# Kernel tuning notes

Hardware: AMD Instinct MI355X
Metric: run time of the kernel (lower is better)

## Reference

```python
import jax, jax.numpy as jnp
import numpy as np

B, T, V, F = 8, 12, 2048, 16
K_CHEB, C = 3, 64

def setup_inputs() -> dict:
    key = jax.random.key(0)
    k1, k2, k3, k4 = jax.random.split(key, 4)
    x = jax.random.normal(k1, (B, T, V, F), dtype=jnp.float32)
    Att = jax.random.uniform(k2, (B, V, V), dtype=jnp.float32)
    cheb = jax.random.normal(k3, (K_CHEB, V, V), dtype=jnp.float32) / np.sqrt(V)
    theta = jax.random.normal(k4, (K_CHEB, F, C), dtype=jnp.float32) * 0.05
    return {"x": x, "Att": Att, "cheb": cheb, "theta": theta}

def reference(x, Att, cheb, theta):
    # Attention-masked Chebyshev polynomials: S_k[b,u,v] = T_k[u,v] * Att[b,u,v]
    # (dropout from the original training-time call is omitted: eval mode)
    masked = cheb[:, None, :, :] * Att[None, :, :, :]            # (K,B,V,V)
    # rhs[b,v,f] = sum_u S_k[b,u,v] * x[b,t,u,f]  (transpose+batch_dot)
    rhs = jnp.einsum('kbuv,btuf->kbtvf', masked, x)              # (K,B,T,V,F)
    # sum over Chebyshev order k of rhs @ Theta_k, then relu
    out = jnp.einsum('kbtvf,kfc->btvc', rhs, theta)              # (B,T,V,C)
    return jax.nn.relu(out)
```

## Files before the change

kernel.cpp:

```cpp
#include <hip/hip_runtime.h>
#include <hip/hip_bf16.h>
#include <stdint.h>

#define B_  8
#define T_  12
#define V_  2048
#define F_  16
#define K_  3
#define C_  64
#define N_  192

typedef _Float16 f16;
typedef _Float16 half4v __attribute__((ext_vector_type(4)));
typedef _Float16 half8v __attribute__((ext_vector_type(8)));
typedef float    f32x4  __attribute__((ext_vector_type(4)));
typedef float    f32x16 __attribute__((ext_vector_type(16)));
typedef unsigned int u32;

__global__ __launch_bounds__(256) void prep_xt(const float* __restrict__ x,
                                               f16* __restrict__ XT) {
  int bid = blockIdx.x;
  int bt = bid >> 2, uc = bid & 3;
  int b = bt / T_, t = bt % T_;
  __shared__ float tile[64][17];
  int r  = threadIdx.x >> 2, fq = threadIdx.x & 3;
  int f  = threadIdx.x >> 4, uq = threadIdx.x & 15;
  for (int u0 = uc * 512; u0 < uc * 512 + 512; u0 += 64) {
    f32x4 v = *(const f32x4*)(x + ((size_t)(b * T_ + t) * V_ + u0 + r) * F_ + fq * 4);
    tile[r][fq * 4 + 0] = v[0];
    tile[r][fq * 4 + 1] = v[1];
    tile[r][fq * 4 + 2] = v[2];
    tile[r][fq * 4 + 3] = v[3];
    __syncthreads();
    half4v h;
    h[0] = (f16)tile[uq * 4 + 0][f];
    h[1] = (f16)tile[uq * 4 + 1][f];
    h[2] = (f16)tile[uq * 4 + 2][f];
    h[3] = (f16)tile[uq * 4 + 3][f];
    *(half4v*)(XT + (size_t)(b * N_ + t * F_ + f) * V_ + u0 + uq * 4) = h;
    __syncthreads();
  }
}

__global__ __launch_bounds__(256) void gemm_kbv(const float* __restrict__ Att,
                                                const float* __restrict__ cheb,
                                                const f16* __restrict__ XT,
                                                f16* __restrict__ rhs) {
  const int vt = blockIdx.x & 31;
  const int kb = blockIdx.x >> 5;
  const int k = kb >> 3, b = kb & 7;
  const int vbase = vt * 64;

  __shared__ char smem[32768];
  char* Ab = smem;
  char* Bb = smem + 8192;

  const int tid = threadIdx.x;
  const int wave = tid >> 6, lane = tid & 63;
  const int wm = wave >> 1, wn = wave & 1;
  const int vsub = (tid & 15) * 4, usub = (tid >> 4) * 4;

  f32x16 acc[3];
  acc[0] = 0; acc[1] = 0; acc[2] = 0;

  for (int u0 = 0; u0 < V_; u0 += 64) {
    __syncthreads();
    const float* cp = cheb + ((size_t)k * V_ + u0 + usub) * V_ + vbase + vsub;
    const float* ap = Att  + ((size_t)b * V_ + u0 + usub) * V_ + vbase + vsub;
    f32x4 p[4];
#pragma unroll
    for (int i = 0; i < 4; ++i) {
      f32x4 cv = *(const f32x4*)(cp + (size_t)i * V_);
      f32x4 av = *(const f32x4*)(ap + (size_t)i * V_);
      p[i] = cv * av;
    }
#pragma unroll
    for (int j = 0; j < 4; ++j) {
      int vrow = vsub + j;
      half4v h;
      h[0] = (f16)p[0][j]; h[1] = (f16)p[1][j];
      h[2] = (f16)p[2][j]; h[3] = (f16)p[3][j];
      *(half4v*)(Ab + vrow * 128 + ((usub * 2) ^ ((vrow & 7) << 4))) = h;
    }
#pragma unroll
    for (int e = 0; e < 6; ++e) {
      int slot = wave * 6 + e;
      int n = slot * 8 + (lane >> 3);
      int cp2 = lane & 7;
      int c = cp2 ^ (n & 7);
      const f16* src = XT + (size_t)(b * N_ + n) * V_ + u0 + c * 8;
      __builtin_amdgcn_global_load_lds((const __attribute__((address_space(1))) u32*)src,
                                       (__attribute__((address_space(3))) u32*)(Bb + slot * 1024),
                                       16, 0, 0);
    }
    __syncthreads();
#pragma unroll
    for (int ks = 0; ks < 4; ++ks) {
      int koff = ks * 32 + (lane >> 5) * 16;
      int vrow = wm * 32 + (lane & 31);
      half8v a = *(const half8v*)(Ab + vrow * 128 + (koff ^ ((vrow & 7) << 4)));
#pragma unroll
      for (int nf = 0; nf < 3; ++nf) {
        int nrow = wn * 96 + nf * 32 + (lane & 31);
        half8v bv = *(const half8v*)(Bb + nrow * 128 + (koff ^ ((nrow & 7) << 4)));
        acc[nf] = __builtin_amdgcn_mfma_f32_32x32x16_f16(a, bv, acc[nf], 0, 0, 0);
      }
    }
  }

#pragma unroll
  for (int nf = 0; nf < 3; ++nf) {
    int n = wn * 96 + nf * 32 + (lane & 31);
    int t = n >> 4, fi = n & 15;
#pragma unroll
    for (int r = 0; r < 16; ++r) {
      int v = vbase + wm * 32 + (r & 3) + 8 * (r >> 2) + 4 * (lane >> 5);
      rhs[((size_t)(b * T_ + t) * V_ + v) * 48 + k * 16 + fi] = (f16)acc[nf][r];
    }
  }
}

__global__ __launch_bounds__(256) void epi(const f16* __restrict__ rhs,
                                           const float* __restrict__ theta,
                                           float* __restrict__ out) {
  int wave = threadIdx.x >> 6, lane = threadIdx.x & 63;
  int row0 = blockIdx.x * 128 + wave * 32;
  int cl = lane & 31, kh = (lane >> 5) * 8;

  half8v bf[2][3];
#pragma unroll
  for (int nf = 0; nf < 2; ++nf)
#pragma unroll
    for (int ks = 0; ks < 3; ++ks) {
      half8v hb;
#pragma unroll
      for (int j = 0; j < 8; ++j)
        hb[j] = (f16)theta[(size_t)(ks * 16 + kh + j) * C_ + nf * 32 + cl];
      bf[nf][ks] = hb;
    }

  f32x16 acc0 = 0, acc1 = 0;
#pragma unroll
  for (int ks = 0; ks < 3; ++ks) {
    half8v a = *(const half8v*)(rhs + (size_t)(row0 + cl) * 48 + ks * 16 + kh);
    acc0 = __builtin_amdgcn_mfma_f32_32x32x16_f16(a, bf[0][ks], acc0, 0, 0, 0);
    acc1 = __builtin_amdgcn_mfma_f32_32x32x16_f16(a, bf[1][ks], acc1, 0, 0, 0);
  }
#pragma unroll
  for (int r = 0; r < 16; ++r) {
    int row = row0 + (r & 3) + 8 * (r >> 2) + 4 * (lane >> 5);
    out[(size_t)row * C_ + cl]      = fmaxf(acc0[r], 0.f);
    out[(size_t)row * C_ + 32 + cl] = fmaxf(acc1[r], 0.f);
  }
}

extern "C" void kernel_launch(void* const* d_in, const int* in_sizes, int n_in,
                              void* d_out, int out_size, void* d_ws, size_t ws_size,
                              hipStream_t stream) {
  const float* x     = (const float*)d_in[0];
  const float* Att   = (const float*)d_in[1];
  const float* cheb  = (const float*)d_in[2];
  const float* theta = (const float*)d_in[3];
  float* out = (float*)d_out;

  f16* XT  = (f16*)d_ws;
  f16* rhs = (f16*)((char*)d_ws + (size_t)B_ * N_ * V_ * sizeof(f16));

  prep_xt<<<B_ * T_ * 4, 256, 0, stream>>>(x, XT);
  gemm_kbv<<<K_ * B_ * 32, 256, 0, stream>>>(Att, cheb, XT, rhs);
  epi<<<(B_ * T_ * V_) / 128, 256, 0, stream>>>(rhs, theta, out);
}
```

Measured before the change: 115.8 us.

## Double-buffer LDS tiles and prefetch next u-chunk during MFMA in gemm_kbv

Converts the main GEMM loop into a two-stage software pipeline. LDS doubles to 64KB so the next chunk's cheb/Att loads and XT global_load_lds run while the current chunk's MFMAs execute, leaving one barrier per iteration. It also reorders the block index so b is the fastest-varying dimension, which may improve L2 reuse of cheb across batches, and raises wave priority around the MFMA section. The larger LDS footprint and extra registers can lower occupancy.

```diff
diff --git a/kernel.cpp b/kernel.cpp
--- a/kernel.cpp
+++ b/kernel.cpp
@@ -46,66 +46,114 @@
                                                 const float* __restrict__ cheb,
                                                 const f16* __restrict__ XT,
                                                 f16* __restrict__ rhs) {
-  const int vt = blockIdx.x & 31;
-  const int kb = blockIdx.x >> 5;
-  const int k = kb >> 3, b = kb & 7;
+  const int bid = blockIdx.x;
+  const int b = bid & 7;
+  const int r2 = bid >> 3;
+  const int vt = r2 & 31, k = r2 >> 5;
   const int vbase = vt * 64;
 
-  __shared__ char smem[32768];
-  char* Ab = smem;
-  char* Bb = smem + 8192;
+  __shared__ char smem[65536];
 
   const int tid = threadIdx.x;
   const int wave = tid >> 6, lane = tid & 63;
   const int wm = wave >> 1, wn = wave & 1;
   const int vsub = (tid & 15) * 4, usub = (tid >> 4) * 4;
 
+  const float* cheb_base = cheb + (size_t)k * V_ * V_ + vbase + vsub + (size_t)usub * V_;
+  const float* att_base  = Att  + (size_t)b * V_ * V_ + vbase + vsub + (size_t)usub * V_;
+  const f16*   xt_base   = XT + (size_t)b * N_ * V_;
+
   f32x16 acc[3];
   acc[0] = 0; acc[1] = 0; acc[2] = 0;
 
-  for (int u0 = 0; u0 < V_; u0 += 64) {
-    __syncthreads();
-    const float* cp = cheb + ((size_t)k * V_ + u0 + usub) * V_ + vbase + vsub;
-    const float* ap = Att  + ((size_t)b * V_ + u0 + usub) * V_ + vbase + vsub;
-    f32x4 p[4];
-#pragma unroll
-    for (int i = 0; i < 4; ++i) {
-      f32x4 cv = *(const f32x4*)(cp + (size_t)i * V_);
-      f32x4 av = *(const f32x4*)(ap + (size_t)i * V_);
-      p[i] = cv * av;
-    }
+  f32x4 pc[4], pa[4];
+
+#pragma unroll
+  for (int i = 0; i < 4; ++i) {
+    pc[i] = *(const f32x4*)(cheb_base + (size_t)i * V_);
+    pa[i] = *(const f32x4*)(att_base  + (size_t)i * V_);
+  }
+  {
+    char* Bb = smem + 8192;
+#pragma unroll
+    for (int e = 0; e < 6; ++e) {
+      int slot = wave * 6 + e;
+      int n = slot * 8 + (lane >> 3);
+      int c = (lane & 7) ^ (n & 7);
+      const f16* src = xt_base + (size_t)n * V_ + c * 8;
+      __builtin_amdgcn_global_load_lds((const __attribute__((address_space(1))) u32*)src,
+                                       (__attribute__((address_space(3))) u32*)(Bb + slot * 1024),
+                                       16, 0, 0);
+    }
+    char* Ab = smem;
 #pragma unroll
     for (int j = 0; j < 4; ++j) {
       int vrow = vsub + j;
       half4v h;
-      h[0] = (f16)p[0][j]; h[1] = (f16)p[1][j];
-      h[2] = (f16)p[2][j]; h[3] = (f16)p[3][j];
+      h[0] = (f16)(pc[0][j] * pa[0][j]); h[1] = (f16)(pc[1][j] * pa[1][j]);
+      h[2] = (f16)(pc[2][j] * pa[2][j]); h[3] = (f16)(pc[3][j] * pa[3][j]);
       *(half4v*)(Ab + vrow * 128 + ((usub * 2) ^ ((vrow & 7) << 4))) = h;
     }
-#pragma unroll
-    for (int e = 0; e < 6; ++e) {
-      int slot = wave * 6 + e;
-      int n = slot * 8 + (lane >> 3);
-      int cp2 = lane & 7;
-      int c = cp2 ^ (n & 7);
-      const f16* src = XT + (size_t)(b * N_ + n) * V_ + u0 + c * 8;
-      __builtin_amdgcn_global_load_lds((const __attribute__((address_space(1))) u32*)src,
-                                       (__attribute__((address_space(3))) u32*)(Bb + slot * 1024),
-                                       16, 0, 0);
+  }
+  __syncthreads();
+
+  int cur = 0;
+  for (int t = 0; t < 32; ++t) {
+    char* bufc = smem + cur * 32768;
+    char* bufn = smem + (cur ^ 1) * 32768;
+
+    if (t < 31) {
+      const size_t uoff = (size_t)(t + 1) * 64 * V_;
+#pragma unroll
+      for (int i = 0; i < 4; ++i) {
+        pc[i] = *(const f32x4*)(cheb_base + uoff + (size_t)i * V_);
+        pa[i] = *(const f32x4*)(att_base  + uoff + (size_t)i * V_);
+      }
+      char* Bb = bufn + 8192;
+#pragma unroll
+      for (int e = 0; e < 6; ++e) {
+        int slot = wave * 6 + e;
+        int n = slot * 8 + (lane >> 3);
+        int c = (lane & 7) ^ (n & 7);
+        const f16* src = xt_base + (size_t)n * V_ + (t + 1) * 64 + c * 8;
+        __builtin_amdgcn_global_load_lds((const __attribute__((address_space(1))) u32*)src,
+                                         (__attribute__((address_space(3))) u32*)(Bb + slot * 1024),
+                                         16, 0, 0);
+      }
+    }
+
+    {
+      char* Ab = bufc;
+      char* Bb = bufc + 8192;
+      __builtin_amdgcn_s_setprio(1);
+#pragma unroll
+      for (int ks = 0; ks < 4; ++ks) {
+        int koff = ks * 32 + (lane >> 5) * 16;
+        int vrow = wm * 32 + (lane & 31);
+        half8v a = *(const half8v*)(Ab + vrow * 128 + (koff ^ ((vrow & 7) << 4)));
+#pragma unroll
+        for (int nf = 0; nf < 3; ++nf) {
+          int nrow = wn * 96 + nf * 32 + (lane & 31);
+          half8v bv = *(const half8v*)(Bb + nrow * 128 + (koff ^ ((nrow & 7) << 4)));
+          acc[nf] = __builtin_amdgcn_mfma_f32_32x32x16_f16(a, bv, acc[nf], 0, 0, 0);
+        }
+      }
+      __builtin_amdgcn_s_setprio(0);
+    }
+
+    if (t < 31) {
+      char* Ab = bufn;
+#pragma unroll
+      for (int j = 0; j < 4; ++j) {
+        int vrow = vsub + j;
+        half4v h;
+        h[0] = (f16)(pc[0][j] * pa[0][j]); h[1] = (f16)(pc[1][j] * pa[1][j]);
+        h[2] = (f16)(pc[2][j] * pa[2][j]); h[3] = (f16)(pc[3][j] * pa[3][j]);
+        *(half4v*)(Ab + vrow * 128 + ((usub * 2) ^ ((vrow & 7) << 4))) = h;
+      }
     }
     __syncthreads();
-#pragma unroll
-    for (int ks = 0; ks < 4; ++ks) {
-      int koff = ks * 32 + (lane >> 5) * 16;
-      int vrow = wm * 32 + (lane & 31);
-      half8v a = *(const half8v*)(Ab + vrow * 128 + (koff ^ ((vrow & 7) << 4)));
-#pragma unroll
-      for (int nf = 0; nf < 3; ++nf) {
-        int nrow = wn * 96 + nf * 32 + (lane & 31);
-        half8v bv = *(const half8v*)(Bb + nrow * 128 + (koff ^ ((nrow & 7) << 4)));
-        acc[nf] = __builtin_amdgcn_mfma_f32_32x32x16_f16(a, bv, acc[nf], 0, 0, 0);
-      }
-    }
+    cur ^= 1;
   }
 
 #pragma unroll
```

After: 140.3 us. +21.1%, slower.

## Fuse Chebyshev orders per block, split-K over u, and software-pipeline loads

Applied to the files above, without the earlier changes.

The GEMM kernel now handles all three Chebyshev orders in one block, so each Att tile and each XT tile is loaded once and reused across k instead of three times. The reduction over u is split into halves across blocks for parallelism. The epilogue sums the partials, which doubles the rhs intermediate. Next-step global loads are prefetched into registers during MFMA work, with setprio around the MFMA bursts. This raises register and LDS use (9 accumulators, 48KB LDS) and may cut occupancy.

```diff
diff --git a/kernel.cpp b/kernel.cpp
--- a/kernel.cpp
+++ b/kernel.cpp
@@ -42,84 +42,169 @@
   }
 }
 
-__global__ __launch_bounds__(256) void gemm_kbv(const float* __restrict__ Att,
-                                                const float* __restrict__ cheb,
-                                                const f16* __restrict__ XT,
-                                                f16* __restrict__ rhs) {
-  const int vt = blockIdx.x & 31;
-  const int kb = blockIdx.x >> 5;
-  const int k = kb >> 3, b = kb & 7;
+template<int UH>
+__global__ __launch_bounds__(256, 2) void gemm_fused(const float* __restrict__ Att,
+                                                     const float* __restrict__ cheb,
+                                                     const f16* __restrict__ XT,
+                                                     f16* __restrict__ rhs) {
+  constexpr int NSTEP = (V_ / UH) / 64;
+  const int bid = blockIdx.x;
+  const int b  = bid / (32 * UH);
+  const int rr = bid % (32 * UH);
+  const int vt = rr / UH, uh = rr % UH;
   const int vbase = vt * 64;
-
-  __shared__ char smem[32768];
+  const size_t ubase = (size_t)uh * (V_ / UH);
+
+  __shared__ char smem[49152];
   char* Ab = smem;
-  char* Bb = smem + 8192;
+  char* Bb = smem + 24576;
 
   const int tid = threadIdx.x;
   const int wave = tid >> 6, lane = tid & 63;
   const int wm = wave >> 1, wn = wave & 1;
   const int vsub = (tid & 15) * 4, usub = (tid >> 4) * 4;
 
-  f32x16 acc[3];
-  acc[0] = 0; acc[1] = 0; acc[2] = 0;
-
-  for (int u0 = 0; u0 < V_; u0 += 64) {
-    __syncthreads();
-    const float* cp = cheb + ((size_t)k * V_ + u0 + usub) * V_ + vbase + vsub;
-    const float* ap = Att  + ((size_t)b * V_ + u0 + usub) * V_ + vbase + vsub;
-    f32x4 p[4];
-#pragma unroll
-    for (int i = 0; i < 4; ++i) {
-      f32x4 cv = *(const f32x4*)(cp + (size_t)i * V_);
-      f32x4 av = *(const f32x4*)(ap + (size_t)i * V_);
-      p[i] = cv * av;
-    }
-#pragma unroll
-    for (int j = 0; j < 4; ++j) {
-      int vrow = vsub + j;
-      half4v h;
-      h[0] = (f16)p[0][j]; h[1] = (f16)p[1][j];
-      h[2] = (f16)p[2][j]; h[3] = (f16)p[3][j];
-      *(half4v*)(Ab + vrow * 128 + ((usub * 2) ^ ((vrow & 7) << 4))) = h;
-    }
+  const float* attb  = Att + (size_t)b * V_ * V_ + vbase + vsub + (size_t)usub * V_;
+  const float* chebb = cheb + vbase + vsub + (size_t)usub * V_;
+  const f16*   xtb   = XT + (size_t)b * N_ * V_;
+
+  f32x16 acc[3][3];
+#pragma unroll
+  for (int k = 0; k < 3; ++k)
+#pragma unroll
+    for (int nf = 0; nf < 3; ++nf) acc[k][nf] = 0;
+
+  const int vrow = wm * 32 + (lane & 31);
+  const int akey = ((vrow >> 2) & 7) << 4;
+  int nrowA[3], bkeyA[3];
+#pragma unroll
+  for (int nf = 0; nf < 3; ++nf) {
+    nrowA[nf] = wn * 96 + nf * 32 + (lane & 31);
+    bkeyA[nf] = (nrowA[nf] & 7) << 4;
+  }
+  const int wkey = (tid & 7) << 4;
+  const int gl_c = (lane & 7) ^ (lane >> 3);
+
+  auto stageB = [&](size_t u) {
 #pragma unroll
     for (int e = 0; e < 6; ++e) {
       int slot = wave * 6 + e;
       int n = slot * 8 + (lane >> 3);
-      int cp2 = lane & 7;
-      int c = cp2 ^ (n & 7);
-      const f16* src = XT + (size_t)(b * N_ + n) * V_ + u0 + c * 8;
+      const f16* src = xtb + (size_t)n * V_ + u + gl_c * 8;
       __builtin_amdgcn_global_load_lds((const __attribute__((address_space(1))) u32*)src,
                                        (__attribute__((address_space(3))) u32*)(Bb + slot * 1024),
                                        16, 0, 0);
     }
-    __syncthreads();
-#pragma unroll
-    for (int ks = 0; ks < 4; ++ks) {
-      int koff = ks * 32 + (lane >> 5) * 16;
-      int vrow = wm * 32 + (lane & 31);
-      half8v a = *(const half8v*)(Ab + vrow * 128 + (koff ^ ((vrow & 7) << 4)));
-#pragma unroll
-      for (int nf = 0; nf < 3; ++nf) {
-        int nrow = wn * 96 + nf * 32 + (lane & 31);
-        half8v bv = *(const half8v*)(Bb + nrow * 128 + (koff ^ ((nrow & 7) << 4)));
-        acc[nf] = __builtin_amdgcn_mfma_f32_32x32x16_f16(a, bv, acc[nf], 0, 0, 0);
+  };
+  auto writeA = [&](half4v pk[3][4]) {
+#pragma unroll
+    for (int k = 0; k < 3; ++k)
+#pragma unroll
+      for (int j = 0; j < 4; ++j)
+        *(half4v*)(Ab + k * 8192 + (vsub + j) * 128 + ((usub * 2) ^ wkey)) = pk[k][j];
+  };
+
+  {
+    f32x4 pa[4], cv[3][4];
+#pragma unroll
+    for (int i = 0; i < 4; ++i) pa[i] = *(const f32x4*)(attb + (ubase + i) * V_);
+#pragma unroll
+    for (int k = 0; k < 3; ++k)
+#pragma unroll
+      for (int i = 0; i < 4; ++i)
+        cv[k][i] = *(const f32x4*)(chebb + (size_t)k * V_ * V_ + (ubase + i) * V_);
+    stageB(ubase);
+    half4v pk[3][4];
+#pragma unroll
+    for (int k = 0; k < 3; ++k)
+#pragma unroll
+      for (int j = 0; j < 4; ++j) {
+        half4v h;
+        h[0] = (f16)(cv[k][0][j] * pa[0][j]); h[1] = (f16)(cv[k][1][j] * pa[1][j]);
+        h[2] = (f16)(cv[k][2][j] * pa[2][j]); h[3] = (f16)(cv[k][3][j] * pa[3][j]);
+        pk[k][j] = h;
       }
-    }
-  }
+    writeA(pk);
+    __syncthreads();
+  }
+
+#define COMPUTE_KS(ks)                                                          \
+  {                                                                             \
+    const int ku2 = (ks) * 32 + (lane >> 5) * 16;                               \
+    half8v bfr0 = *(const half8v*)(Bb + nrowA[0] * 128 + (ku2 ^ bkeyA[0]));     \
+    half8v bfr1 = *(const half8v*)(Bb + nrowA[1] * 128 + (ku2 ^ bkeyA[1]));     \
+    half8v bfr2 = *(const half8v*)(Bb + nrowA[2] * 128 + (ku2 ^ bkeyA[2]));     \
+    __builtin_amdgcn_s_setprio(1);                                              \
+    _Pragma("unroll")                                                           \
+    for (int k = 0; k < 3; ++k) {                                               \
+      half8v a = *(const half8v*)(Ab + k * 8192 + vrow * 128 + (ku2 ^ akey));   \
+      acc[k][0] = __builtin_amdgcn_mfma_f32_32x32x16_f16(a, bfr0, acc[k][0], 0, 0, 0); \
+      acc[k][1] = __builtin_amdgcn_mfma_f32_32x32x16_f16(a, bfr1, acc[k][1], 0, 0, 0); \
+      acc[k][2] = __builtin_amdgcn_mfma_f32_32x32x16_f16(a, bfr2, acc[k][2], 0, 0, 0); \
+    }                                                                           \
+    __builtin_amdgcn_s_setprio(0);                                              \
+  }
+
+  for (int t = 0; t < NSTEP; ++t) {
+    const bool pref = (t + 1) < NSTEP;
+    const size_t unext = ubase + (size_t)(t + 1) * 64;
+    f32x4 pa[4], cv[3][4];
+    half4v pk[3][4];
+
+    if (pref) {
+#pragma unroll
+      for (int i = 0; i < 4; ++i) pa[i] = *(const f32x4*)(attb + (unext + i) * V_);
+#pragma unroll
+      for (int k = 0; k < 3; ++k)
+#pragma unroll
+        for (int i = 0; i < 4; ++i)
+          cv[k][i] = *(const f32x4*)(chebb + (size_t)k * V_ * V_ + (unext + i) * V_);
+    }
+
+    COMPUTE_KS(0)
+    COMPUTE_KS(1)
+
+    if (pref) {
+#pragma unroll
+      for (int k = 0; k < 3; ++k)
+#pragma unroll
+        for (int j = 0; j < 4; ++j) {
+          half4v h;
+          h[0] = (f16)(cv[k][0][j] * pa[0][j]); h[1] = (f16)(cv[k][1][j] * pa[1][j]);
+          h[2] = (f16)(cv[k][2][j] * pa[2][j]); h[3] = (f16)(cv[k][3][j] * pa[3][j]);
+          pk[k][j] = h;
+        }
+    }
+
+    COMPUTE_KS(2)
+    COMPUTE_KS(3)
+
+    __syncthreads();
+    if (pref) {
+      stageB(unext);
+      writeA(pk);
+      __syncthreads();
+    }
+  }
+#undef COMPUTE_KS
 
 #pragma unroll
   for (int nf = 0; nf < 3; ++nf) {
     int n = wn * 96 + nf * 32 + (lane & 31);
-    int t = n >> 4, fi = n & 15;
-#pragma unroll
-    for (int r = 0; r < 16; ++r) {
-      int v = vbase + wm * 32 + (r & 3) + 8 * (r >> 2) + 4 * (lane >> 5);
-      rhs[((size_t)(b * T_ + t) * V_ + v) * 48 + k * 16 + fi] = (f16)acc[nf][r];
-    }
-  }
-}
-
+    int tt = n >> 4, fi = n & 15;
+#pragma unroll
+    for (int k = 0; k < 3; ++k) {
+#pragma unroll
+      for (int r = 0; r < 16; ++r) {
+        int v = vbase + wm * 32 + (r & 3) + 8 * (r >> 2) + 4 * (lane >> 5);
+        rhs[((size_t)(b * T_ + tt) * V_ + v) * (48 * UH) + uh * 48 + k * 16 + fi] =
+            (f16)acc[k][nf][r];
+      }
+    }
+  }
+}
+
+template<int UH>
 __global__ __launch_bounds__(256) void epi(const f16* __restrict__ rhs,
                                            const float* __restrict__ theta,
                                            float* __restrict__ out) {
@@ -141,10 +226,10 @@
 
   f32x16 acc0 = 0, acc1 = 0;
 #pragma unroll
-  for (int ks = 0; ks < 3; ++ks) {
-    half8v a = *(const half8v*)(rhs + (size_t)(row0 + cl) * 48 + ks * 16 + kh);
-    acc0 = __builtin_amdgcn_mfma_f32_32x32x16_f16(a, bf[0][ks], acc0, 0, 0, 0);
-    acc1 = __builtin_amdgcn_mfma_f32_32x32x16_f16(a, bf[1][ks], acc1, 0, 0, 0);
+  for (int s = 0; s < 3 * UH; ++s) {
+    half8v a = *(const half8v*)(rhs + (size_t)(row0 + cl) * (48 * UH) + s * 16 + kh);
+    acc0 = __builtin_amdgcn_mfma_f32_32x32x16_f16(a, bf[0][s % 3], acc0, 0, 0, 0);
+    acc1 = __builtin_amdgcn_mfma_f32_32x32x16_f16(a, bf[1][s % 3], acc1, 0, 0, 0);
   }
 #pragma unroll
   for (int r = 0; r < 16; ++r) {
@@ -163,10 +248,18 @@
   const float* theta = (const float*)d_in[3];
   float* out = (float*)d_out;
 
+  const size_t xtB   = (size_t)B_ * N_ * V_ * sizeof(f16);
+  const size_t rhsB2 = (size_t)B_ * T_ * V_ * 96 * sizeof(f16);
+
   f16* XT  = (f16*)d_ws;
-  f16* rhs = (f16*)((char*)d_ws + (size_t)B_ * N_ * V_ * sizeof(f16));
+  f16* rhs = (f16*)((char*)d_ws + xtB);
 
   prep_xt<<<B_ * T_ * 4, 256, 0, stream>>>(x, XT);
-  gemm_kbv<<<K_ * B_ * 32, 256, 0, stream>>>(Att, cheb, XT, rhs);
-  epi<<<(B_ * T_ * V_) / 128, 256, 0, stream>>>(rhs, theta, out);
-}
+  if (ws_size >= xtB + rhsB2) {
+    gemm_fused<2><<<B_ * 32 * 2, 256, 0, stream>>>(Att, cheb, XT, rhs);
+    epi<2><<<(B_ * T_ * V_) / 128, 256, 0, stream>>>(rhs, theta, out);
+  } else {
+    gemm_fused<1><<<B_ * 32, 256, 0, stream>>>(Att, cheb, XT, rhs);
+    epi<1><<<(B_ * T_ * V_) / 128, 256, 0, stream>>>(rhs, theta, out);
+  }
+}
```

After: 107.2 us. 7.5% less time.

## Share Att tiles across Chebyshev orders with split-U double-buffered GEMM

Applied to the files above, without the earlier changes.

The GEMM is restructured so each block loads its Att tile once and reuses it for all three Chebyshev orders, holding nine accumulators instead of three, which removes the threefold re-reading of Att. Cheb is pre-converted by a new kernel into an f16 layout that matches the MFMA register fragments, and is read straight from global memory and multiplied with the Att fragment in registers. The U dimension is split across two blocks and the partial sums are reduced in the epilogue GEMM, and the LDS staging is double-buffered so loads overlap with MFMA work. In exchange there is an extra prep pass over cheb, a larger workspace, and higher register and LDS pressure that limit occupancy.

```diff
diff --git a/kernel.cpp b/kernel.cpp
--- a/kernel.cpp
+++ b/kernel.cpp
@@ -42,84 +42,192 @@
   }
 }
 
-__global__ __launch_bounds__(256) void gemm_kbv(const float* __restrict__ Att,
-                                                const float* __restrict__ cheb,
+__global__ __launch_bounds__(256) void prep_chebT(const float* __restrict__ c,
+                                                  f16* __restrict__ cT) {
+  int bid = blockIdx.x;
+  int vt = bid & 31, ut = (bid >> 5) & 31, k = bid >> 10;
+  int u0 = ut * 64, v0 = vt * 64;
+  __shared__ float tile[64][68];
+  int tid = threadIdx.x;
+  int lr = tid >> 4, lc = (tid & 15) * 4;
+  const float* src = c + ((size_t)k * V_ + u0) * V_ + v0;
+#pragma unroll
+  for (int i = 0; i < 4; ++i) {
+    f32x4 v = *(const f32x4*)(src + (size_t)(lr + 16 * i) * V_ + lc);
+    tile[lr + 16 * i][lc + 0] = v[0];
+    tile[lr + 16 * i][lc + 1] = v[1];
+    tile[lr + 16 * i][lc + 2] = v[2];
+    tile[lr + 16 * i][lc + 3] = v[3];
+  }
+  __syncthreads();
+  int vl = tid & 63, uc0 = tid >> 6;
+#pragma unroll
+  for (int i = 0; i < 2; ++i) {
+    int uc = uc0 + 4 * i;
+    half8v h;
+#pragma unroll
+    for (int j = 0; j < 8; ++j) h[j] = (f16)tile[uc * 8 + j][vl];
+    int vb = (v0 + vl) >> 5;
+    int vi = vl & 31;
+    size_t ut_idx = (size_t)(u0 >> 3) + uc;
+    size_t off = ((((size_t)k * 64 + vb) * 256 + ut_idx) * 32 + vi) * 8;
+    *(half8v*)(cT + off) = h;
+  }
+}
+
+#define MFMA_H(a, b, c) __builtin_amdgcn_mfma_f32_32x32x16_f16(a, b, c, 0, 0, 0)
+
+#define KS_GROUP(ks, AC, BC)                                                   \
+  {                                                                            \
+    const int kb = (ks) * 32 + hi * 16;                                        \
+    half8v af = *(const half8v*)((AC) + vrow * 128 + (kb ^ skey));             \
+    half8v b0 = *(const half8v*)((BC) + nrow0 * 128 + (kb ^ bk0));             \
+    half8v b1 = *(const half8v*)((BC) + nrow1 * 128 + (kb ^ bk1));             \
+    half8v b2 = *(const half8v*)((BC) + nrow2 * 128 + (kb ^ bk2));             \
+    const size_t co = (size_t)(t * 8 + (ks) * 2 + hi) * 256;                   \
+    half8v c0 = *(const half8v*)(chb0 + co);                                   \
+    half8v c1 = *(const half8v*)(chb1 + co);                                   \
+    half8v c2 = *(const half8v*)(chb2 + co);                                   \
+    half8v a0 = c0 * af, a1 = c1 * af, a2 = c2 * af;                           \
+    __builtin_amdgcn_s_setprio(1);                                             \
+    acc[0][0] = MFMA_H(a0, b0, acc[0][0]);                                     \
+    acc[0][1] = MFMA_H(a0, b1, acc[0][1]);                                     \
+    acc[0][2] = MFMA_H(a0, b2, acc[0][2]);                                     \
+    acc[1][0] = MFMA_H(a1, b0, acc[1][0]);                                     \
+    acc[1][1] = MFMA_H(a1, b1, acc[1][1]);                                     \
+    acc[1][2] = MFMA_H(a1, b2, acc[1][2]);                                     \
+    acc[2][0] = MFMA_H(a2, b0, acc[2][0]);                                     \
+    acc[2][1] = MFMA_H(a2, b1, acc[2][1]);                                     \
+    acc[2][2] = MFMA_H(a2, b2, acc[2][2]);                                     \
+    __builtin_amdgcn_s_setprio(0);                                             \
+  }
+
+template<int UH>
+__global__ __launch_bounds__(256, 2) void gemm2(const float* __restrict__ Att,
+                                                const f16* __restrict__ chebT,
                                                 const f16* __restrict__ XT,
                                                 f16* __restrict__ rhs) {
-  const int vt = blockIdx.x & 31;
-  const int kb = blockIdx.x >> 5;
-  const int k = kb >> 3, b = kb & 7;
+  constexpr int NSTEP = (V_ / UH) / 64;
+  const int bid = blockIdx.x;
+  const int vt = bid & 31;
+  const int rr = bid >> 5;
+  const int b  = rr / UH;
+  const int uh = rr % UH;
   const int vbase = vt * 64;
-
-  __shared__ char smem[32768];
-  char* Ab = smem;
-  char* Bb = smem + 8192;
+  const size_t ubase = (size_t)uh * (V_ / UH);
+
+  __shared__ char smem[65536];
+  char* Bb0 = smem;
+  char* Bb1 = smem + 24576;
+  char* Ab0 = smem + 49152;
+  char* Ab1 = smem + 57344;
 
   const int tid = threadIdx.x;
   const int wave = tid >> 6, lane = tid & 63;
   const int wm = wave >> 1, wn = wave & 1;
+  const int hi = lane >> 5, l31 = lane & 31;
+  const int vrow = wm * 32 + l31;
   const int vsub = (tid & 15) * 4, usub = (tid >> 4) * 4;
 
-  f32x16 acc[3];
-  acc[0] = 0; acc[1] = 0; acc[2] = 0;
-
-  for (int u0 = 0; u0 < V_; u0 += 64) {
-    __syncthreads();
-    const float* cp = cheb + ((size_t)k * V_ + u0 + usub) * V_ + vbase + vsub;
-    const float* ap = Att  + ((size_t)b * V_ + u0 + usub) * V_ + vbase + vsub;
-    f32x4 p[4];
-#pragma unroll
-    for (int i = 0; i < 4; ++i) {
-      f32x4 cv = *(const f32x4*)(cp + (size_t)i * V_);
-      f32x4 av = *(const f32x4*)(ap + (size_t)i * V_);
-      p[i] = cv * av;
-    }
-#pragma unroll
-    for (int j = 0; j < 4; ++j) {
-      int vrow = vsub + j;
-      half4v h;
-      h[0] = (f16)p[0][j]; h[1] = (f16)p[1][j];
-      h[2] = (f16)p[2][j]; h[3] = (f16)p[3][j];
-      *(half4v*)(Ab + vrow * 128 + ((usub * 2) ^ ((vrow & 7) << 4))) = h;
-    }
+  const int skey = ((vrow + (vrow >> 3)) & 7) << 4;
+  const int nrow0 = wn * 96 + l31;
+  const int nrow1 = nrow0 + 32;
+  const int nrow2 = nrow0 + 64;
+  const int bk0 = (nrow0 & 7) << 4, bk1 = (nrow1 & 7) << 4, bk2 = (nrow2 & 7) << 4;
+
+  const int vb = vt * 2 + wm;
+  const f16* chb0 = chebT + (((size_t)vb * 256 + (ubase >> 3)) * 32 + l31) * 8;
+  const f16* chb1 = chb0 + (size_t)V_ * V_;
+  const f16* chb2 = chb1 + (size_t)V_ * V_;
+
+  const float* attb = Att + (size_t)b * V_ * V_ + (ubase + usub) * V_ + vbase + vsub;
+  const f16*   xtb  = XT + (size_t)b * N_ * V_ + ubase;
+
+  f32x16 acc[3][3];
+#pragma unroll
+  for (int k = 0; k < 3; ++k)
+#pragma unroll
+    for (int nf = 0; nf < 3; ++nf) acc[k][nf] = 0;
+
+  f32x4 pa[4];
+  const int gl_c = lane & 7;
+
+  auto stageB = [&](int t, char* Bb) {
 #pragma unroll
     for (int e = 0; e < 6; ++e) {
       int slot = wave * 6 + e;
       int n = slot * 8 + (lane >> 3);
-      int cp2 = lane & 7;
-      int c = cp2 ^ (n & 7);
-      const f16* src = XT + (size_t)(b * N_ + n) * V_ + u0 + c * 8;
+      int cc = gl_c ^ (n & 7);
+      const f16* src = xtb + (size_t)n * V_ + t * 64 + cc * 8;
       __builtin_amdgcn_global_load_lds((const __attribute__((address_space(1))) u32*)src,
                                        (__attribute__((address_space(3))) u32*)(Bb + slot * 1024),
                                        16, 0, 0);
     }
-    __syncthreads();
-#pragma unroll
-    for (int ks = 0; ks < 4; ++ks) {
-      int koff = ks * 32 + (lane >> 5) * 16;
-      int vrow = wm * 32 + (lane & 31);
-      half8v a = *(const half8v*)(Ab + vrow * 128 + (koff ^ ((vrow & 7) << 4)));
-#pragma unroll
-      for (int nf = 0; nf < 3; ++nf) {
-        int nrow = wn * 96 + nf * 32 + (lane & 31);
-        half8v bv = *(const half8v*)(Bb + nrow * 128 + (koff ^ ((nrow & 7) << 4)));
-        acc[nf] = __builtin_amdgcn_mfma_f32_32x32x16_f16(a, bv, acc[nf], 0, 0, 0);
+  };
+  auto issueAtt = [&](int t) {
+#pragma unroll
+    for (int i = 0; i < 4; ++i)
+      pa[i] = *(const f32x4*)(attb + (size_t)(t * 64 + i) * V_);
+  };
+  auto writeAtt = [&](char* Aw) {
+#pragma unroll
+    for (int j = 0; j < 4; ++j) {
+      int vr = vsub + j;
+      half4v h;
+      h[0] = (f16)pa[0][j]; h[1] = (f16)pa[1][j];
+      h[2] = (f16)pa[2][j]; h[3] = (f16)pa[3][j];
+      *(half4v*)(Aw + vr * 128 + ((usub * 2) ^ (((vr + (vr >> 3)) & 7) << 4))) = h;
+    }
+  };
+
+  issueAtt(0);
+  stageB(0, Bb0);
+  writeAtt(Ab0);
+  __syncthreads();
+
+#pragma unroll 1
+  for (int t0 = 0; t0 < NSTEP; t0 += 2) {
+    {
+      const int t = t0;
+      issueAtt(t + 1);
+      stageB(t + 1, Bb1);
+      KS_GROUP(0, Ab0, Bb0)
+      KS_GROUP(1, Ab0, Bb0)
+      KS_GROUP(2, Ab0, Bb0)
+      KS_GROUP(3, Ab0, Bb0)
+      writeAtt(Ab1);
+      __syncthreads();
+    }
+    {
+      const int t = t0 + 1;
+      const bool p2 = (t + 1) < NSTEP;
+      if (p2) { issueAtt(t + 1); stageB(t + 1, Bb0); }
+      KS_GROUP(0, Ab1, Bb1)
+      KS_GROUP(1, Ab1, Bb1)
+      KS_GROUP(2, Ab1, Bb1)
+      KS_GROUP(3, Ab1, Bb1)
+      if (p2) writeAtt(Ab0);
+      __syncthreads();
+    }
+  }
+
+#pragma unroll
+  for (int nf = 0; nf < 3; ++nf) {
+    int n = wn * 96 + nf * 32 + l31;
+    int tt = n >> 4, fi = n & 15;
+#pragma unroll
+    for (int k = 0; k < 3; ++k) {
+#pragma unroll
+      for (int r = 0; r < 16; ++r) {
+        int v = vbase + wm * 32 + (r & 3) + 8 * (r >> 2) + 4 * hi;
+        rhs[((size_t)(b * T_ + tt) * V_ + v) * (48 * UH) + uh * 48 + k * 16 + fi] =
+            (f16)acc[k][nf][r];
       }
     }
   }
-
-#pragma unroll
-  for (int nf = 0; nf < 3; ++nf) {
-    int n = wn * 96 + nf * 32 + (lane & 31);
-    int t = n >> 4, fi = n & 15;
-#pragma unroll
-    for (int r = 0; r < 16; ++r) {
-      int v = vbase + wm * 32 + (r & 3) + 8 * (r >> 2) + 4 * (lane >> 5);
-      rhs[((size_t)(b * T_ + t) * V_ + v) * 48 + k * 16 + fi] = (f16)acc[nf][r];
-    }
-  }
-}
-
+}
+
+template<int UH>
 __global__ __launch_bounds__(256) void epi(const f16* __restrict__ rhs,
                                            const float* __restrict__ theta,
                                            float* __restrict__ out) {
@@ -141,10 +249,10 @@
 
   f32x16 acc0 = 0, acc1 = 0;
 #pragma unroll
-  for (int ks = 0; ks < 3; ++ks) {
-    half8v a = *(const half8v*)(rhs + (size_t)(row0 + cl) * 48 + ks * 16 + kh);
-    acc0 = __builtin_amdgcn_mfma_f32_32x32x16_f16(a, bf[0][ks], acc0, 0, 0, 0);
-    acc1 = __builtin_amdgcn_mfma_f32_32x32x16_f16(a, bf[1][ks], acc1, 0, 0, 0);
+  for (int s = 0; s < 3 * UH; ++s) {
+    half8v a = *(const half8v*)(rhs + (size_t)(row0 + cl) * (48 * UH) + s * 16 + kh);
+    acc0 = __builtin_amdgcn_mfma_f32_32x32x16_f16(a, bf[0][s % 3], acc0, 0, 0, 0);
+    acc1 = __builtin_amdgcn_mfma_f32_32x32x16_f16(a, bf[1][s % 3], acc1, 0, 0, 0);
   }
 #pragma unroll
   for (int r = 0; r < 16; ++r) {
@@ -163,10 +271,25 @@
   const float* theta = (const float*)d_in[3];
   float* out = (float*)d_out;
 
-  f16* XT  = (f16*)d_ws;
-  f16* rhs = (f16*)((char*)d_ws + (size_t)B_ * N_ * V_ * sizeof(f16));
-
+  const size_t xtB   = (size_t)B_ * N_ * V_ * sizeof(f16);
+  const size_t rhs2B = (size_t)B_ * T_ * V_ * 96 * sizeof(f16);
+  const size_t rhs1B = rhs2B / 2;
+  const size_t chB   = (size_t)K_ * V_ * V_ * sizeof(f16);
+
+  f16* XT = (f16*)d_ws;
   prep_xt<<<B_ * T_ * 4, 256, 0, stream>>>(x, XT);
-  gemm_kbv<<<K_ * B_ * 32, 256, 0, stream>>>(Att, cheb, XT, rhs);
-  epi<<<(B_ * T_ * V_) / 128, 256, 0, stream>>>(rhs, theta, out);
-}
+
+  if (ws_size >= xtB + rhs2B + chB) {
+    f16* rhs = (f16*)((char*)d_ws + xtB);
+    f16* cT  = (f16*)((char*)d_ws + xtB + rhs2B);
+    prep_chebT<<<K_ * 32 * 32, 256, 0, stream>>>(cheb, cT);
+    gemm2<2><<<B_ * 32 * 2, 256, 0, stream>>>(Att, cT, XT, rhs);
+    epi<2><<<(B_ * T_ * V_) / 128, 256, 0, stream>>>(rhs, theta, out);
+  } else {
+    f16* rhs = (f16*)((char*)d_ws + xtB);
+    f16* cT  = (f16*)((char*)d_ws + xtB + rhs1B);
+    prep_chebT<<<K_ * 32 * 32, 256, 0, stream>>>(cheb, cT);
+    gemm2<1><<<B_ * 32, 256, 0, stream>>>(Att, cT, XT, rhs);
+    epi<1><<<(B_ * T_ * V_) / 128, 256, 0, stream>>>(rhs, theta, out);
+  }
+}
```

New measurement: 112.6 us. -2.8%, faster.
